# Performance work log

Hardware: AMD Instinct MI355X
Metric: run time of the kernel (lower is better)

## Reference

```python
import jax, jax.numpy as jnp
import numpy as np

H = 128          # LSTMCell hidden size (fixed in module)
D_IN = 128       # input_dim
D_PROJ = 256     # input_layer output / LSTM input size
LAYER_NUM = 2
DA = 128
R = 8
OUT_DIM = 7
B = 256
T = 512
TS = 32          # time_steps


def _lstm_cell(h, c, x_t, W_ih, b_ih, W_hh, b_hh):
    # PyTorch LSTMCell gate order: i, f, g, o
    gates = x_t @ W_ih.T + h @ W_hh.T + (b_ih + b_hh)
    i, f, g, o = jnp.split(gates, 4, axis=-1)
    c_new = jax.nn.sigmoid(f) * c + jax.nn.sigmoid(i) * jnp.tanh(g)
    h_new = jax.nn.sigmoid(o) * jnp.tanh(c_new)
    return h_new, c_new


def _chunked_lstm(x_tbd, W_ih, b_ih, W_hh, b_hh, w_time, time_steps):
    # x_tbd: [T, B, 256]. Every `time_steps` steps, h/c are replaced by a
    # learned linear reweighting (time_w_layer) of the buffered chunk states;
    # the chunk's last emitted output is the reweighted h (as in the source).
    Tt, Bb, Dd = x_tbd.shape

    def cell_step(carry, x_t):
        h, c = carry
        h, c = _lstm_cell(h, c, x_t, W_ih, b_ih, W_hh, b_hh)
        return (h, c), (h, c)

    def chunk_step(carry, x_chunk):        # x_chunk: [ts, B, 256]
        _, (hs, cs) = jax.lax.scan(cell_step, carry, x_chunk)  # hs: [ts, B, H]
        h_new = jnp.einsum('t,tbh->bh', w_time, hs)
        c_new = jnp.einsum('t,tbh->bh', w_time, cs)
        return (h_new, c_new), hs.at[-1].set(h_new)

    n_chunks = Tt // time_steps
    x_chunks = x_tbd.reshape(n_chunks, time_steps, Bb, Dd)
    h0 = jnp.zeros((Bb, H), x_tbd.dtype)
    _, outs = jax.lax.scan(chunk_step, (h0, jnp.zeros_like(h0)), x_chunks)
    return outs.reshape(Tt, Bb, H)


def setup_inputs() -> dict:
    key = jax.random.key(0)
    ks = jax.random.split(key, 16)
    def unif(k, shape, fan_in):
        bound = 1.0 / np.sqrt(fan_in)
        return jax.random.uniform(k, shape, jnp.float32, -bound, bound)
    inp = {
        'x': jax.random.normal(ks[0], (B, T, D_IN), jnp.float32),
        'W_in': unif(ks[1], (D_PROJ, D_IN), D_IN),
        'b_in': unif(ks[2], (D_PROJ,), D_IN),
        'W_ih': unif(ks[3], (4 * H, D_PROJ), H),
        'b_ih': unif(ks[4], (4 * H,), H),
        'W_hh': unif(ks[5], (4 * H, H), H),
        'b_hh': unif(ks[6], (4 * H,), H),
        'w_time': unif(ks[7], (TS,), TS),
        'W_a1': unif(ks[8], (DA, 2 * H), 2 * H),
        'b_a1': unif(ks[9], (DA,), 2 * H),
        'W_a2': unif(ks[10], (R, DA), DA),
        'W_out': unif(ks[11], (OUT_DIM, 2 * H * R), 2 * H * R),
        'b_out': unif(ks[12], (OUT_DIM,), 2 * H * R),
        'length': jax.random.randint(ks[13], (B,), T // 2, T + 1),
        'batch_size': B,
        'time_steps': TS,
        'r': R,
    }
    return inp


def reference(x, W_in, b_in, W_ih, b_ih, W_hh, b_hh, w_time, W_a1, b_a1,
              W_a2, W_out, b_out, length, batch_size, time_steps, r):
    Bb, Tt, _ = x.shape
    out = x @ W_in.T + b_in                       # [B, T, 256]
    for _ in range(LAYER_NUM):                    # shared LSTM weights per source
        inp = jnp.transpose(out, (1, 0, 2))       # [T, B, 256]
        out1 = _chunked_lstm(inp, W_ih, b_ih, W_hh, b_hh, w_time, time_steps)
        out2 = _chunked_lstm(inp[::-1], W_ih, b_ih, W_hh, b_hh, w_time, time_steps)
        # NOTE: backward outputs are NOT re-reversed (faithful to source)
        out = jnp.transpose(jnp.concatenate([out1, out2], axis=-1), (1, 0, 2))
    # attention (dropout = identity at eval)
    pot = jnp.tanh(out @ W_a1.T + b_a1) @ W_a2.T  # [B, T, r]
    mask = (jnp.arange(Tt)[None, :] < length[:, None])[:, :, None]
    logits = jnp.where(mask, pot, -jnp.inf)
    weight = jnp.where(mask, jax.nn.softmax(logits, axis=1), 0.0)  # [B, T, r]
    wT = jnp.transpose(weight, (0, 2, 1))          # [B, r, T]
    pooled = jnp.einsum('brt,bth->brh', wT, out).reshape(Bb, -1)   # [B, r*256]
    out_final = jax.nn.log_softmax(pooled @ W_out.T + b_out, axis=1)
    sw = jnp.sqrt(wT)
    gram = jnp.einsum('brt,bst->brs', sw, sw)      # [B, r, r]
    penalty = jnp.sum((gram - 1.0) ** 2)           # oneMat is all-ones
    return out_final, penalty
```

## Files before the change

### kernel.cpp

```cpp
#include <hip/hip_runtime.h>
#include <math.h>

namespace {

constexpr int Bb = 256, Tt = 512, Dp = 256, Hh = 128, G = 512;
constexpr int M = Tt * Bb;

typedef __attribute__((ext_vector_type(8))) short short8v;
typedef __attribute__((ext_vector_type(4))) float f32x4;

__device__ __forceinline__ float sigf(float x) {
  return __builtin_amdgcn_rcpf(1.0f + __expf(-x));
}
__device__ __forceinline__ float tanhfast(float x) {
  const float e = __expf(2.0f * x);
  return 1.0f - 2.0f * __builtin_amdgcn_rcpf(e + 1.0f);
}
__device__ __forceinline__ float b2f(unsigned short u) {
  return __uint_as_float((unsigned int)u << 16);
}
__device__ __forceinline__ unsigned short f2b(float f) {
  unsigned int u = __float_as_uint(f);
  u += 0x7FFFu + ((u >> 16) & 1u);
  return (unsigned short)(u >> 16);
}
__device__ __forceinline__ unsigned int pack2(float a, float b) {
  return (unsigned int)f2b(a) | ((unsigned int)f2b(b) << 16);
}
__device__ __forceinline__ void gload16(const unsigned short* g, unsigned short* l) {
  __builtin_amdgcn_global_load_lds(
      (const __attribute__((address_space(1))) unsigned int*)g,
      (__attribute__((address_space(3))) unsigned int*)l, 16, 0, 0);
}
__device__ __forceinline__ void block_sync_lds() {
  __builtin_amdgcn_sched_barrier(0);
  asm volatile("s_waitcnt lgkmcnt(0)" ::: "memory");
  __builtin_amdgcn_s_barrier();
  __builtin_amdgcn_sched_barrier(0);
}

__global__ __launch_bounds__(256) void wconv_k(const float* __restrict__ src,
                                               unsigned short* __restrict__ dst) {
  const int i = (blockIdx.x * 256 + threadIdx.x) * 4;
  const float4 v = *reinterpret_cast<const float4*>(src + i);
  uint2 o; o.x = pack2(v.x, v.y); o.y = pack2(v.z, v.w);
  *reinterpret_cast<uint2*>(dst + i) = o;
}

__global__ __launch_bounds__(256) void xconv_k(const float* __restrict__ x,
                                               unsigned short* __restrict__ out) {
  const int tid = threadIdx.x;
  const int m = blockIdx.x * 8 + (tid >> 5);
  const int t = m >> 8, b = m & 255;
  const int c4 = (tid & 31) * 4;
  const float4 v = *reinterpret_cast<const float4*>(x + ((size_t)b * Tt + t) * 128 + c4);
  uint2 o; o.x = pack2(v.x, v.y); o.y = pack2(v.z, v.w);
  *reinterpret_cast<uint2*>(out + (size_t)m * 128 + c4) = o;
}

template<int K, int POT, typename CT>
__global__ __launch_bounds__(256) void mgemm_k(const unsigned short* __restrict__ A,
    const unsigned short* __restrict__ W, const float* __restrict__ bias1,
    const float* __restrict__ bias2, const float* __restrict__ Wa2,
    CT* __restrict__ C, int N) {
  constexpr int NK = K / 64;
  __shared__ unsigned short smem[32768];
  unsigned short* aLds = smem;
  unsigned short* wLds = smem + 16384;
  const int tid = threadIdx.x;
  const int lane = tid & 63;
  const int wave = tid >> 6;
  const int wm = wave >> 1, wn = wave & 1;
  const int m0 = blockIdx.y * 128, n0 = blockIdx.x * 128;
  const int lrow = lane & 15, lk8 = (lane >> 4) * 8;

  const unsigned short* Ab = A + (size_t)(m0 + lrow) * K + lk8;
  const unsigned short* Wb = W + (size_t)(n0 + lrow) * K + lk8;

  auto stage = [&](int buf, int kb) {
#pragma unroll
    for (int i = 0; i < 4; ++i) {
      const int c = wave * 4 + i, f = c & 7, kc = c >> 3;
      const size_t go = (size_t)(f * 16) * K + kb * 64 + kc * 32;
      gload16(Ab + go, &aLds[buf * 8192 + c * 512]);
      gload16(Wb + go, &wLds[buf * 8192 + c * 512]);
    }
  };

  f32x4 acc[4][4] = {};
  stage(0, 0);
  __syncthreads();
  int cur = 0;
  for (int kb = 0; kb < NK; ++kb) {
    if (kb + 1 < NK) stage(cur ^ 1, kb + 1);
#pragma unroll
    for (int kc = 0; kc < 2; ++kc) {
      short8v af[4], bfr[4];
#pragma unroll
      for (int i = 0; i < 4; ++i)
        af[i] = *reinterpret_cast<const short8v*>(
            &aLds[cur * 8192 + ((kc * 8 + wm * 4 + i) * 64 + lane) * 8]);
#pragma unroll
      for (int j = 0; j < 4; ++j)
        bfr[j] = *reinterpret_cast<const short8v*>(
            &wLds[cur * 8192 + ((kc * 8 + wn * 4 + j) * 64 + lane) * 8]);
#pragma unroll
      for (int i = 0; i < 4; ++i)
#pragma unroll
        for (int j = 0; j < 4; ++j)
          acc[i][j] = __builtin_amdgcn_mfma_f32_16x16x32_bf16(af[i], bfr[j], acc[i][j], 0, 0, 0);
    }
    __syncthreads();
    cur ^= 1;
  }

  if constexpr (POT) {
    unsigned short* pt = smem;
#pragma unroll
    for (int j = 0; j < 4; ++j) {
      const int coln = wn * 64 + j * 16 + (lane & 15);
      const float bv = bias1[coln];
#pragma unroll
      for (int i = 0; i < 4; ++i) {
        const int rown = wm * 64 + i * 16 + ((lane >> 4) << 2);
#pragma unroll
        for (int r = 0; r < 4; ++r)
          pt[(rown + r) * 136 + coln] = f2b(tanhfast(acc[i][j][r] + bv));
      }
    }
    __syncthreads();
    short8v wfr[4];
#pragma unroll
    for (int ks = 0; ks < 4; ++ks) {
      short8v f = {0, 0, 0, 0, 0, 0, 0, 0};
      if (lrow < 8) {
        const float* src = Wa2 + lrow * 128 + ks * 32 + lk8;
        const float4 a = *reinterpret_cast<const float4*>(src);
        const float4 b = *reinterpret_cast<const float4*>(src + 4);
        f[0] = (short)f2b(a.x); f[1] = (short)f2b(a.y);
        f[2] = (short)f2b(a.z); f[3] = (short)f2b(a.w);
        f[4] = (short)f2b(b.x); f[5] = (short)f2b(b.y);
        f[6] = (short)f2b(b.z); f[7] = (short)f2b(b.w);
      }
      wfr[ks] = f;
    }
    float* pot = reinterpret_cast<float*>(C);
#pragma unroll
    for (int ff = 0; ff < 2; ++ff) {
      const int fr = wave * 2 + ff;
      f32x4 pacc = {0.f, 0.f, 0.f, 0.f};
#pragma unroll
      for (int ks = 0; ks < 4; ++ks) {
        const short8v af = *reinterpret_cast<const short8v*>(
            &pt[(fr * 16 + lrow) * 136 + ks * 32 + lk8]);
        pacc = __builtin_amdgcn_mfma_f32_16x16x32_bf16(af, wfr[ks], pacc, 0, 0, 0);
      }
      if ((lane & 15) < 8) {
#pragma unroll
        for (int r = 0; r < 4; ++r)
          pot[(size_t)(m0 + fr * 16 + ((lane >> 4) << 2) + r) * 8 + (lane & 15)] = pacc[r];
      }
    }
  } else {
#pragma unroll
    for (int j = 0; j < 4; ++j) {
      const int gn = n0 + wn * 64 + j * 16 + (lane & 15);
      float bv = bias1[gn];
      if (bias2) bv += bias2[gn];
#pragma unroll
      for (int i = 0; i < 4; ++i) {
        const int gmb = m0 + wm * 64 + i * 16 + ((lane >> 4) << 2);
#pragma unroll
        for (int r = 0; r < 4; ++r) {
          const float v = acc[i][j][r] + bv;
          const size_t oidx = (size_t)(gmb + r) * N + gn;
          if constexpr (sizeof(CT) == 2) C[oidx] = f2b(v); else C[oidx] = v;
        }
      }
    }
  }
}

__global__ __launch_bounds__(512, 2) void lstm_k(const unsigned short* __restrict__ P,
    const float* __restrict__ Whh, const float* __restrict__ wtime,
    unsigned short* __restrict__ Y) {
  const int tid = threadIdx.x;
  const int lane = tid & 63;
  const int w = tid >> 6;
  const int u = lane & 15;
  const int q = lane >> 4;
  const int dir = blockIdx.x >> 7;
  const int b0 = (blockIdx.x & 127) * 2;

  __shared__ unsigned short hbuf[2][2048];
  __shared__ unsigned int pgbuf[2][512];
  __shared__ unsigned short histb[4096];
  __shared__ float wts[32];

  short8v bfrag[4][4];
#pragma unroll
  for (int gt = 0; gt < 4; ++gt) {
    const int col = gt * 128 + w * 16 + u;
#pragma unroll
    for (int ks = 0; ks < 4; ++ks) {
      const int k0 = ks * 32 + q * 8;
      const float4 w0 = *reinterpret_cast<const float4*>(Whh + (size_t)col * 128 + k0);
      const float4 w1 = *reinterpret_cast<const float4*>(Whh + (size_t)col * 128 + k0 + 4);
      short8v f;
      f[0] = (short)f2b(w0.x); f[1] = (short)f2b(w0.y);
      f[2] = (short)f2b(w0.z); f[3] = (short)f2b(w0.w);
      f[4] = (short)f2b(w1.x); f[5] = (short)f2b(w1.y);
      f[6] = (short)f2b(w1.z); f[7] = (short)f2b(w1.w);
      bfrag[gt][ks] = f;
    }
  }

  for (int i = tid; i < 2048; i += 512) { hbuf[0][i] = 0; hbuf[1][i] = 0; }
  if (tid < 32) wts[tid] = wtime[tid];
  const unsigned int* P32 = reinterpret_cast<const unsigned int*>(P);
  const int prow = tid >> 8, pword = tid & 255;
  const size_t pthread = (size_t)(b0 + prow) * 256 + pword;
  const ptrdiff_t dstep = (dir ? -(ptrdiff_t)1 : (ptrdiff_t)1) * (ptrdiff_t)(Bb * 256);
  unsigned int np_h1 = 0, np_h2 = 0;
  {
    const int t0 = dir ? (Tt - 1) : 0;
    pgbuf[0][tid] = P32[(size_t)t0 * Bb * 256 + pthread];
    const int t1 = dir ? (Tt - 2) : 1;
    np_h1 = P32[(size_t)t1 * Bb * 256 + pthread];
    const int t2 = dir ? (Tt - 3) : 2;
    np_h2 = P32[(size_t)t2 * Bb * 256 + pthread];
  }
  ptrdiff_t poff = (ptrdiff_t)((size_t)(dir ? (Tt - 4) : 3) * Bb * 256 + pthread);
  const int r_own = q & 1;
  const int colh = w * 16 + u;
  float c_st = 0.f, ha = 0.f, ca = 0.f;
  __syncthreads();

  auto body = [&](int s, int cur) {
    unsigned int np_new = 0;
    if (s < Tt - 3) np_new = P32[poff];
    short8v afrag[4];
#pragma unroll
    for (int ks = 0; ks < 4; ++ks)
      afrag[ks] = *reinterpret_cast<const short8v*>(&hbuf[cur][(ks * 4 + q) * 128 + u * 8]);
    f32x4 gacc[4];
#pragma unroll
    for (int gt = 0; gt < 4; ++gt) {
      f32x4 acc = {0.f, 0.f, 0.f, 0.f};
#pragma unroll
      for (int ks = 0; ks < 4; ++ks)
        acc = __builtin_amdgcn_mfma_f32_16x16x32_bf16(afrag[ks], bfrag[gt][ks], acc, 0, 0, 0);
      gacc[gt] = acc;
    }
    if (s + 1 < Tt) pgbuf[cur ^ 1][tid] = np_h1;
    if (lane < 32) {
      const float wt = wts[s & 31];
      float g4[4];
#pragma unroll
      for (int gt = 0; gt < 4; ++gt) {
        const unsigned int pw = pgbuf[cur][r_own * 256 + gt * 64 + (colh >> 1)];
        const unsigned short pb = (colh & 1) ? (unsigned short)(pw >> 16)
                                             : (unsigned short)(pw & 0xFFFF);
        g4[gt] = gacc[gt][0] + b2f(pb);
      }
      float cs = sigf(g4[1]) * c_st + sigf(g4[0]) * tanhfast(g4[2]);
      float hn = sigf(g4[3]) * tanhfast(cs);
      ha += wt * hn;
      ca += wt * cs;
      if ((s & 31) == 31) { hn = ha; cs = ca; ha = 0.f; ca = 0.f; }
      c_st = cs;
      const unsigned short hb = f2b(hn);
      hbuf[cur ^ 1][(colh >> 3) * 128 + r_own * 32 + (colh & 7)] = hb;
      histb[((s & 15) * 2 + r_own) * 128 + colh] = hb;
    }
    if ((s & 7) == 0 && s) {
      const int k = tid >> 6, r2 = (tid >> 5) & 1, c4 = (tid & 31) * 4;
      const int bs = s - 8;
      const uint2 v = *reinterpret_cast<const uint2*>(
          &histb[(((bs + k) & 15) * 2 + r2) * 128 + c4]);
      *reinterpret_cast<uint2*>(
          &Y[((size_t)(bs + k) * Bb + b0 + r2) * Dp + dir * Hh + c4]) = v;
    }
    block_sync_lds();
    np_h1 = np_h2;
    np_h2 = np_new;
    poff += dstep;
  };

  for (int s = 0; s < Tt; s += 2) {
    body(s, 0);
    body(s + 1, 1);
  }
  {
    const int k = tid >> 6, r2 = (tid >> 5) & 1, c4 = (tid & 31) * 4;
    const int bs = Tt - 8;
    const uint2 v = *reinterpret_cast<const uint2*>(
        &histb[(((bs + k) & 15) * 2 + r2) * 128 + c4]);
    *reinterpret_cast<uint2*>(
        &Y[((size_t)(bs + k) * Bb + b0 + r2) * Dp + dir * Hh + c4]) = v;
  }
}

__global__ __launch_bounds__(256) void softmax_k(const float* __restrict__ pot,
    const int* __restrict__ length, float* __restrict__ Wt) {
  const int b = blockIdx.x >> 3, r = blockIdx.x & 7;
  const int tid = threadIdx.x;
  const int len = length[b];
  __shared__ float rbuf[4];
  const int t1 = tid, t2 = tid + 256;
  const float x1 = (t1 < len) ? pot[((size_t)t1 * Bb + b) * 8 + r] : -INFINITY;
  const float x2 = (t2 < len) ? pot[((size_t)t2 * Bb + b) * 8 + r] : -INFINITY;
  float m = fmaxf(x1, x2);
#pragma unroll
  for (int off = 32; off >= 1; off >>= 1) m = fmaxf(m, __shfl_xor(m, off));
  if ((tid & 63) == 0) rbuf[tid >> 6] = m;
  __syncthreads();
  m = fmaxf(fmaxf(rbuf[0], rbuf[1]), fmaxf(rbuf[2], rbuf[3]));
  const float e1 = (t1 < len) ? __expf(x1 - m) : 0.f;
  const float e2 = (t2 < len) ? __expf(x2 - m) : 0.f;
  float ssum = e1 + e2;
#pragma unroll
  for (int off = 32; off >= 1; off >>= 1) ssum += __shfl_xor(ssum, off);
  __syncthreads();
  if ((tid & 63) == 0) rbuf[tid >> 6] = ssum;
  __syncthreads();
  ssum = rbuf[0] + rbuf[1] + rbuf[2] + rbuf[3];
  const float inv = 1.0f / ssum;
  float* wrow = Wt + ((size_t)b * 8 + r) * Tt;
  wrow[t1] = e1 * inv;
  wrow[t2] = e2 * inv;
}

__global__ __launch_bounds__(256) void pool_k(const unsigned short* __restrict__ Y,
    const float* __restrict__ Wt, const float* __restrict__ Wout,
    const float* __restrict__ bout, float* __restrict__ outF,
    float* __restrict__ penpart) {
  const int b = blockIdx.x;
  const int tid = threadIdx.x;
  __shared__ float ws[8 * 513];
  __shared__ float pooled[2048];
  __shared__ float red[256];
  __shared__ float lg[8];
  for (int i = tid; i < 4096; i += 256) ws[(i >> 9) * 513 + (i & 511)] = Wt[(size_t)b * 4096 + i];
  __syncthreads();
  float acc[8] = {};
  for (int t = 0; t < Tt; ++t) {
    const float y = b2f(Y[((size_t)t * Bb + b) * Dp + tid]);
#pragma unroll
    for (int r = 0; r < 8; ++r) acc[r] += ws[r * 513 + t] * y;
  }
#pragma unroll
  for (int r = 0; r < 8; ++r) pooled[r * 256 + tid] = acc[r];
  __syncthreads();
  for (int o = 0; o < 7; ++o) {
    float p = 0.f;
    for (int j = tid; j < 2048; j += 256) p += pooled[j] * Wout[(size_t)o * 2048 + j];
    red[tid] = p;
    __syncthreads();
    for (int st = 128; st >= 1; st >>= 1) {
      if (tid < st) red[tid] += red[tid + st];
      __syncthreads();
    }
    if (tid == 0) lg[o] = red[0] + bout[o];
    __syncthreads();
  }
  if (tid == 0) {
    float mx = lg[0];
    for (int o = 1; o < 7; ++o) mx = fmaxf(mx, lg[o]);
    float ssum = 0.f;
    for (int o = 0; o < 7; ++o) ssum += __expf(lg[o] - mx);
    const float lse = mx + __logf(ssum);
    for (int o = 0; o < 7; ++o) outF[b * 7 + o] = lg[o] - lse;
  }
  for (int i = tid; i < 4096; i += 256) {
    const int rr = i >> 9, t = i & 511;
    ws[rr * 513 + t] = sqrtf(ws[rr * 513 + t]);
  }
  __syncthreads();
  float pp = 0.f;
  if (tid < 64) {
    const int rr = tid >> 3, ssi = tid & 7;
    float g = 0.f;
    for (int t = 0; t < Tt; ++t) g += ws[rr * 513 + t] * ws[ssi * 513 + t];
    const float d = g - 1.0f;
    pp = d * d;
  }
  red[tid] = pp;
  __syncthreads();
  for (int st = 128; st >= 1; st >>= 1) {
    if (tid < st) red[tid] += red[tid + st];
    __syncthreads();
  }
  if (tid == 0) penpart[b] = red[0];
}

__global__ __launch_bounds__(256) void penred_k(const float* __restrict__ penpart,
                                                float* __restrict__ outp) {
  const int tid = threadIdx.x;
  __shared__ float red[256];
  red[tid] = penpart[tid];
  __syncthreads();
  for (int st = 128; st >= 1; st >>= 1) {
    if (tid < st) red[tid] += red[tid + st];
    __syncthreads();
  }
  if (tid == 0) outp[0] = red[0];
}

}

extern "C" void kernel_launch(void* const* d_in, const int* in_sizes, int n_in,
                              void* d_out, int out_size, void* d_ws, size_t ws_size,
                              hipStream_t stream) {
  (void)in_sizes; (void)n_in; (void)out_size;
  const float* x     = (const float*)d_in[0];
  const float* W_in  = (const float*)d_in[1];
  const float* b_in  = (const float*)d_in[2];
  const float* W_ih  = (const float*)d_in[3];
  const float* b_ih  = (const float*)d_in[4];
  const float* W_hh  = (const float*)d_in[5];
  const float* b_hh  = (const float*)d_in[6];
  const float* wtime = (const float*)d_in[7];
  const float* W_a1  = (const float*)d_in[8];
  const float* b_a1  = (const float*)d_in[9];
  const float* W_a2  = (const float*)d_in[10];
  const float* W_out = (const float*)d_in[11];
  const float* b_out = (const float*)d_in[12];
  const int*   length= (const int*)d_in[13];
  float* outF = (float*)d_out;

  typedef unsigned short bf16;
  char* ws = (char*)d_ws;
  size_t off = 0;
  auto alloc = [&](size_t bytes) {
    void* p = ws + off; off += (bytes + 255) & ~(size_t)255; return p;
  };
  bf16*  act  = (bf16*)alloc((size_t)M * 256 * 2);
  bf16*  Pg   = (bf16*)alloc((size_t)M * 512 * 2);
  bf16*  xb   = (bf16*)alloc((size_t)M * 128 * 2);
  float* pot  = (float*)alloc((size_t)M * 8 * 4);
  float* Wt   = (float*)alloc((size_t)Bb * 8 * Tt * 4);
  float* penp = (float*)alloc(Bb * 4);
  bf16*  Wihb = (bf16*)alloc(512 * 256 * 2);
  bf16*  Winb = (bf16*)alloc(256 * 128 * 2);
  bf16*  Wa1b = (bf16*)alloc(128 * 256 * 2);

  if (ws_size < off) return;

  const dim3 blk(256);
  wconv_k<<<dim3(32),  blk, 0, stream>>>(W_in, Winb);
  wconv_k<<<dim3(128), blk, 0, stream>>>(W_ih, Wihb);
  wconv_k<<<dim3(32),  blk, 0, stream>>>(W_a1, Wa1b);
  xconv_k<<<dim3(M / 8), blk, 0, stream>>>(x, xb);
  mgemm_k<128, 0, bf16><<<dim3(2, M / 128), blk, 0, stream>>>(xb, Winb, b_in, nullptr, nullptr, act, 256);
  mgemm_k<256, 0, bf16><<<dim3(4, M / 128), blk, 0, stream>>>(act, Wihb, b_ih, b_hh, nullptr, Pg, 512);
  lstm_k<<<dim3(256), dim3(512), 0, stream>>>(Pg, W_hh, wtime, act);
  mgemm_k<256, 0, bf16><<<dim3(4, M / 128), blk, 0, stream>>>(act, Wihb, b_ih, b_hh, nullptr, Pg, 512);
  lstm_k<<<dim3(256), dim3(512), 0, stream>>>(Pg, W_hh, wtime, act);
  mgemm_k<256, 1, float><<<dim3(1, M / 128), blk, 0, stream>>>(act, Wa1b, b_a1, nullptr, W_a2, pot, 128);
  softmax_k<<<dim3(Bb * 8), blk, 0, stream>>>(pot, length, Wt);
  pool_k<<<dim3(Bb), blk, 0, stream>>>(act, Wt, W_out, b_out, outF, penp);
  penred_k<<<dim3(1), blk, 0, stream>>>(penp, outF + Bb * 7);
}
```

Baseline: 898.0 us.

## Split LSTM recurrence to one batch row per block, doubling grid size

The recurrent LSTM kernel now handles one batch row per block instead of two, launching 512 blocks rather than 256, and the launch bound is raised to 4 blocks per SU. Per-step LDS buffers shrink, and only the first 16 lanes of each wave do the gate math. The goal is to spread the serial recurrence across more CUs so each block's per-step critical path is shorter. The cost is that every block still runs the full 16x16 MFMA tile while using only one of its rows, and each block reloads the W_hh fragments, so MFMA work and weight loading roughly double. Register pressure under the tighter launch bound could also cause spills.

```diff
diff --git a/kernel.cpp b/kernel.cpp
--- a/kernel.cpp
+++ b/kernel.cpp
@@ -181,7 +181,7 @@
   }
 }
 
-__global__ __launch_bounds__(512, 2) void lstm_k(const unsigned short* __restrict__ P,
+__global__ __launch_bounds__(512, 4) void lstm_k(const unsigned short* __restrict__ P,
     const float* __restrict__ Whh, const float* __restrict__ wtime,
     unsigned short* __restrict__ Y) {
   const int tid = threadIdx.x;
@@ -189,12 +189,12 @@
   const int w = tid >> 6;
   const int u = lane & 15;
   const int q = lane >> 4;
-  const int dir = blockIdx.x >> 7;
-  const int b0 = (blockIdx.x & 127) * 2;
+  const int dir = blockIdx.x >> 8;
+  const int b0 = blockIdx.x & 255;
 
   __shared__ unsigned short hbuf[2][2048];
-  __shared__ unsigned int pgbuf[2][512];
-  __shared__ unsigned short histb[4096];
+  __shared__ unsigned int pgbuf[2][256];
+  __shared__ unsigned short histb[2048];
   __shared__ float wts[32];
 
   short8v bfrag[4][4];
@@ -218,11 +218,11 @@
   for (int i = tid; i < 2048; i += 512) { hbuf[0][i] = 0; hbuf[1][i] = 0; }
   if (tid < 32) wts[tid] = wtime[tid];
   const unsigned int* P32 = reinterpret_cast<const unsigned int*>(P);
-  const int prow = tid >> 8, pword = tid & 255;
-  const size_t pthread = (size_t)(b0 + prow) * 256 + pword;
+  const bool pf = tid < 256;
+  const size_t pthread = (size_t)b0 * 256 + tid;
   const ptrdiff_t dstep = (dir ? -(ptrdiff_t)1 : (ptrdiff_t)1) * (ptrdiff_t)(Bb * 256);
   unsigned int np_h1 = 0, np_h2 = 0;
-  {
+  if (pf) {
     const int t0 = dir ? (Tt - 1) : 0;
     pgbuf[0][tid] = P32[(size_t)t0 * Bb * 256 + pthread];
     const int t1 = dir ? (Tt - 2) : 1;
@@ -231,14 +231,13 @@
     np_h2 = P32[(size_t)t2 * Bb * 256 + pthread];
   }
   ptrdiff_t poff = (ptrdiff_t)((size_t)(dir ? (Tt - 4) : 3) * Bb * 256 + pthread);
-  const int r_own = q & 1;
   const int colh = w * 16 + u;
   float c_st = 0.f, ha = 0.f, ca = 0.f;
   __syncthreads();
 
   auto body = [&](int s, int cur) {
     unsigned int np_new = 0;
-    if (s < Tt - 3) np_new = P32[poff];
+    if (pf && s < Tt - 3) np_new = P32[poff];
     short8v afrag[4];
 #pragma unroll
     for (int ks = 0; ks < 4; ++ks)
@@ -252,13 +251,13 @@
         acc = __builtin_amdgcn_mfma_f32_16x16x32_bf16(afrag[ks], bfrag[gt][ks], acc, 0, 0, 0);
       gacc[gt] = acc;
     }
-    if (s + 1 < Tt) pgbuf[cur ^ 1][tid] = np_h1;
-    if (lane < 32) {
+    if (pf && s + 1 < Tt) pgbuf[cur ^ 1][tid] = np_h1;
+    if (lane < 16) {
       const float wt = wts[s & 31];
       float g4[4];
 #pragma unroll
       for (int gt = 0; gt < 4; ++gt) {
-        const unsigned int pw = pgbuf[cur][r_own * 256 + gt * 64 + (colh >> 1)];
+        const unsigned int pw = pgbuf[cur][gt * 64 + (colh >> 1)];
         const unsigned short pb = (colh & 1) ? (unsigned short)(pw >> 16)
                                              : (unsigned short)(pw & 0xFFFF);
         g4[gt] = gacc[gt][0] + b2f(pb);
@@ -270,16 +269,15 @@
       if ((s & 31) == 31) { hn = ha; cs = ca; ha = 0.f; ca = 0.f; }
       c_st = cs;
       const unsigned short hb = f2b(hn);
-      hbuf[cur ^ 1][(colh >> 3) * 128 + r_own * 32 + (colh & 7)] = hb;
-      histb[((s & 15) * 2 + r_own) * 128 + colh] = hb;
-    }
-    if ((s & 7) == 0 && s) {
-      const int k = tid >> 6, r2 = (tid >> 5) & 1, c4 = (tid & 31) * 4;
+      hbuf[cur ^ 1][(colh >> 3) * 128 + (colh & 7)] = hb;
+      histb[(s & 15) * 128 + colh] = hb;
+    }
+    if ((s & 7) == 0 && s && pf) {
+      const int k = tid >> 5, c4 = (tid & 31) * 4;
       const int bs = s - 8;
-      const uint2 v = *reinterpret_cast<const uint2*>(
-          &histb[(((bs + k) & 15) * 2 + r2) * 128 + c4]);
+      const uint2 v = *reinterpret_cast<const uint2*>(&histb[((bs + k) & 15) * 128 + c4]);
       *reinterpret_cast<uint2*>(
-          &Y[((size_t)(bs + k) * Bb + b0 + r2) * Dp + dir * Hh + c4]) = v;
+          &Y[((size_t)(bs + k) * Bb + b0) * Dp + dir * Hh + c4]) = v;
     }
     block_sync_lds();
     np_h1 = np_h2;
@@ -292,12 +290,13 @@
     body(s + 1, 1);
   }
   {
-    const int k = tid >> 6, r2 = (tid >> 5) & 1, c4 = (tid & 31) * 4;
-    const int bs = Tt - 8;
-    const uint2 v = *reinterpret_cast<const uint2*>(
-        &histb[(((bs + k) & 15) * 2 + r2) * 128 + c4]);
-    *reinterpret_cast<uint2*>(
-        &Y[((size_t)(bs + k) * Bb + b0 + r2) * Dp + dir * Hh + c4]) = v;
+    if (pf) {
+      const int k = tid >> 5, c4 = (tid & 31) * 4;
+      const int bs = Tt - 8;
+      const uint2 v = *reinterpret_cast<const uint2*>(&histb[((bs + k) & 15) * 128 + c4]);
+      *reinterpret_cast<uint2*>(
+          &Y[((size_t)(bs + k) * Bb + b0) * Dp + dir * Hh + c4]) = v;
+    }
   }
 }
 
@@ -454,9 +453,9 @@
   xconv_k<<<dim3(M / 8), blk, 0, stream>>>(x, xb);
   mgemm_k<128, 0, bf16><<<dim3(2, M / 128), blk, 0, stream>>>(xb, Winb, b_in, nullptr, nullptr, act, 256);
   mgemm_k<256, 0, bf16><<<dim3(4, M / 128), blk, 0, stream>>>(act, Wihb, b_ih, b_hh, nullptr, Pg, 512);
-  lstm_k<<<dim3(256), dim3(512), 0, stream>>>(Pg, W_hh, wtime, act);
+  lstm_k<<<dim3(512), dim3(512), 0, stream>>>(Pg, W_hh, wtime, act);
   mgemm_k<256, 0, bf16><<<dim3(4, M / 128), blk, 0, stream>>>(act, Wihb, b_ih, b_hh, nullptr, Pg, 512);
-  lstm_k<<<dim3(256), dim3(512), 0, stream>>>(Pg, W_hh, wtime, act);
+  lstm_k<<<dim3(512), dim3(512), 0, stream>>>(Pg, W_hh, wtime, act);
   mgemm_k<256, 1, float><<<dim3(1, M / 128), blk, 0, stream>>>(act, Wa1b, b_a1, nullptr, W_a2, pot, 128);
   softmax_k<<<dim3(Bb * 8), blk, 0, stream>>>(pot, length, Wt);
   pool_k<<<dim3(Bb), blk, 0, stream>>>(act, Wt, W_out, b_out, outF, penp);
```

New measurement: 1.227 ms. 36.7% more time.

## Halve LSTM block to 4 waves, each computing two 16-column tiles

Applied to the files above, without the earlier changes.

The recurrent LSTM kernel now runs 256 threads per block instead of 512. Each wave keeps W_hh fragments for two 16-column tiles and issues twice as many MFMAs per step, and all 64 lanes do the gate math instead of only half. The aim is to shrink the per-step block barrier and make better use of lanes on the latency-bound serial recurrence. In exchange, each wave holds twice as many register-resident weight fragments, which raises register pressure and lengthens each wave's serial MFMA chain.

```diff
diff --git a/kernel.cpp b/kernel.cpp
--- a/kernel.cpp
+++ b/kernel.cpp
@@ -181,7 +181,7 @@
   }
 }
 
-__global__ __launch_bounds__(512, 2) void lstm_k(const unsigned short* __restrict__ P,
+__global__ __launch_bounds__(256, 2) void lstm_k(const unsigned short* __restrict__ P,
     const float* __restrict__ Whh, const float* __restrict__ wtime,
     unsigned short* __restrict__ Y) {
   const int tid = threadIdx.x;
@@ -197,71 +197,82 @@
   __shared__ unsigned short histb[4096];
   __shared__ float wts[32];
 
-  short8v bfrag[4][4];
-#pragma unroll
-  for (int gt = 0; gt < 4; ++gt) {
-    const int col = gt * 128 + w * 16 + u;
-#pragma unroll
-    for (int ks = 0; ks < 4; ++ks) {
-      const int k0 = ks * 32 + q * 8;
-      const float4 w0 = *reinterpret_cast<const float4*>(Whh + (size_t)col * 128 + k0);
-      const float4 w1 = *reinterpret_cast<const float4*>(Whh + (size_t)col * 128 + k0 + 4);
-      short8v f;
-      f[0] = (short)f2b(w0.x); f[1] = (short)f2b(w0.y);
-      f[2] = (short)f2b(w0.z); f[3] = (short)f2b(w0.w);
-      f[4] = (short)f2b(w1.x); f[5] = (short)f2b(w1.y);
-      f[6] = (short)f2b(w1.z); f[7] = (short)f2b(w1.w);
-      bfrag[gt][ks] = f;
-    }
-  }
-
-  for (int i = tid; i < 2048; i += 512) { hbuf[0][i] = 0; hbuf[1][i] = 0; }
+  short8v bfrag[4][2][4];
+#pragma unroll
+  for (int gt = 0; gt < 4; ++gt)
+#pragma unroll
+    for (int t2 = 0; t2 < 2; ++t2) {
+      const int col = gt * 128 + w * 32 + t2 * 16 + u;
+#pragma unroll
+      for (int ks = 0; ks < 4; ++ks) {
+        const int k0 = ks * 32 + q * 8;
+        const float4 w0 = *reinterpret_cast<const float4*>(Whh + (size_t)col * 128 + k0);
+        const float4 w1 = *reinterpret_cast<const float4*>(Whh + (size_t)col * 128 + k0 + 4);
+        short8v f;
+        f[0] = (short)f2b(w0.x); f[1] = (short)f2b(w0.y);
+        f[2] = (short)f2b(w0.z); f[3] = (short)f2b(w0.w);
+        f[4] = (short)f2b(w1.x); f[5] = (short)f2b(w1.y);
+        f[6] = (short)f2b(w1.z); f[7] = (short)f2b(w1.w);
+        bfrag[gt][t2][ks] = f;
+      }
+    }
+
+  for (int i = tid; i < 2048; i += 256) { hbuf[0][i] = 0; hbuf[1][i] = 0; }
   if (tid < 32) wts[tid] = wtime[tid];
   const unsigned int* P32 = reinterpret_cast<const unsigned int*>(P);
-  const int prow = tid >> 8, pword = tid & 255;
-  const size_t pthread = (size_t)(b0 + prow) * 256 + pword;
-  const ptrdiff_t dstep = (dir ? -(ptrdiff_t)1 : (ptrdiff_t)1) * (ptrdiff_t)(Bb * 256);
-  unsigned int np_h1 = 0, np_h2 = 0;
+  const size_t bstep = (size_t)Bb * 256;
+  const ptrdiff_t pstep = dir ? -(ptrdiff_t)bstep : (ptrdiff_t)bstep;
+  const size_t b0w = (size_t)b0 * 256 + tid;
+  const size_t b1w = (size_t)(b0 + 1) * 256 + tid;
+  ptrdiff_t pt0 = (ptrdiff_t)((size_t)(dir ? (Tt - 1) : 0) * bstep);
+  unsigned int h1a, h1b, h2a, h2b;
   {
-    const int t0 = dir ? (Tt - 1) : 0;
-    pgbuf[0][tid] = P32[(size_t)t0 * Bb * 256 + pthread];
-    const int t1 = dir ? (Tt - 2) : 1;
-    np_h1 = P32[(size_t)t1 * Bb * 256 + pthread];
-    const int t2 = dir ? (Tt - 3) : 2;
-    np_h2 = P32[(size_t)t2 * Bb * 256 + pthread];
-  }
-  ptrdiff_t poff = (ptrdiff_t)((size_t)(dir ? (Tt - 4) : 3) * Bb * 256 + pthread);
-  const int r_own = q & 1;
-  const int colh = w * 16 + u;
+    pgbuf[0][tid] = P32[pt0 + b0w];
+    pgbuf[0][tid + 256] = P32[pt0 + b1w];
+    h1a = P32[pt0 + pstep + b0w];
+    h1b = P32[pt0 + pstep + b1w];
+    h2a = P32[pt0 + 2 * pstep + b0w];
+    h2b = P32[pt0 + 2 * pstep + b1w];
+  }
+  ptrdiff_t poff = pt0 + 3 * pstep;
+  const int t2o = lane >> 5;
+  const int r_own = (lane >> 4) & 1;
+  const int colh = w * 32 + t2o * 16 + u;
   float c_st = 0.f, ha = 0.f, ca = 0.f;
   __syncthreads();
 
   auto body = [&](int s, int cur) {
-    unsigned int np_new = 0;
-    if (s < Tt - 3) np_new = P32[poff];
+    unsigned int na = 0, nb = 0;
+    if (s < Tt - 3) { na = P32[poff + b0w]; nb = P32[poff + b1w]; }
     short8v afrag[4];
 #pragma unroll
     for (int ks = 0; ks < 4; ++ks)
       afrag[ks] = *reinterpret_cast<const short8v*>(&hbuf[cur][(ks * 4 + q) * 128 + u * 8]);
-    f32x4 gacc[4];
-#pragma unroll
-    for (int gt = 0; gt < 4; ++gt) {
-      f32x4 acc = {0.f, 0.f, 0.f, 0.f};
-#pragma unroll
-      for (int ks = 0; ks < 4; ++ks)
-        acc = __builtin_amdgcn_mfma_f32_16x16x32_bf16(afrag[ks], bfrag[gt][ks], acc, 0, 0, 0);
-      gacc[gt] = acc;
-    }
-    if (s + 1 < Tt) pgbuf[cur ^ 1][tid] = np_h1;
-    if (lane < 32) {
+    f32x4 gacc[4][2];
+#pragma unroll
+    for (int gt = 0; gt < 4; ++gt)
+#pragma unroll
+      for (int t2 = 0; t2 < 2; ++t2) {
+        f32x4 acc = {0.f, 0.f, 0.f, 0.f};
+#pragma unroll
+        for (int ks = 0; ks < 4; ++ks)
+          acc = __builtin_amdgcn_mfma_f32_16x16x32_bf16(afrag[ks], bfrag[gt][t2][ks], acc, 0, 0, 0);
+        gacc[gt][t2] = acc;
+      }
+    if (s + 1 < Tt) {
+      pgbuf[cur ^ 1][tid] = h1a;
+      pgbuf[cur ^ 1][tid + 256] = h1b;
+    }
+    {
       const float wt = wts[s & 31];
       float g4[4];
 #pragma unroll
       for (int gt = 0; gt < 4; ++gt) {
+        const float gv = t2o ? gacc[gt][1][0] : gacc[gt][0][0];
         const unsigned int pw = pgbuf[cur][r_own * 256 + gt * 64 + (colh >> 1)];
         const unsigned short pb = (colh & 1) ? (unsigned short)(pw >> 16)
                                              : (unsigned short)(pw & 0xFFFF);
-        g4[gt] = gacc[gt][0] + b2f(pb);
+        g4[gt] = gv + b2f(pb);
       }
       float cs = sigf(g4[1]) * c_st + sigf(g4[0]) * tanhfast(g4[2]);
       float hn = sigf(g4[3]) * tanhfast(cs);
@@ -274,17 +285,17 @@
       histb[((s & 15) * 2 + r_own) * 128 + colh] = hb;
     }
     if ((s & 7) == 0 && s) {
-      const int k = tid >> 6, r2 = (tid >> 5) & 1, c4 = (tid & 31) * 4;
+      const int k = tid >> 5, r2 = (tid >> 4) & 1, c8 = (tid & 15) * 8;
       const int bs = s - 8;
-      const uint2 v = *reinterpret_cast<const uint2*>(
-          &histb[(((bs + k) & 15) * 2 + r2) * 128 + c4]);
-      *reinterpret_cast<uint2*>(
-          &Y[((size_t)(bs + k) * Bb + b0 + r2) * Dp + dir * Hh + c4]) = v;
+      const uint4 v = *reinterpret_cast<const uint4*>(
+          &histb[(((bs + k) & 15) * 2 + r2) * 128 + c8]);
+      *reinterpret_cast<uint4*>(
+          &Y[((size_t)(bs + k) * Bb + b0 + r2) * Dp + dir * Hh + c8]) = v;
     }
     block_sync_lds();
-    np_h1 = np_h2;
-    np_h2 = np_new;
-    poff += dstep;
+    h1a = h2a; h1b = h2b;
+    h2a = na;  h2b = nb;
+    poff += pstep;
   };
 
   for (int s = 0; s < Tt; s += 2) {
@@ -292,12 +303,12 @@
     body(s + 1, 1);
   }
   {
-    const int k = tid >> 6, r2 = (tid >> 5) & 1, c4 = (tid & 31) * 4;
+    const int k = tid >> 5, r2 = (tid >> 4) & 1, c8 = (tid & 15) * 8;
     const int bs = Tt - 8;
-    const uint2 v = *reinterpret_cast<const uint2*>(
-        &histb[(((bs + k) & 15) * 2 + r2) * 128 + c4]);
-    *reinterpret_cast<uint2*>(
-        &Y[((size_t)(bs + k) * Bb + b0 + r2) * Dp + dir * Hh + c4]) = v;
+    const uint4 v = *reinterpret_cast<const uint4*>(
+        &histb[(((bs + k) & 15) * 2 + r2) * 128 + c8]);
+    *reinterpret_cast<uint4*>(
+        &Y[((size_t)(bs + k) * Bb + b0 + r2) * Dp + dir * Hh + c8]) = v;
   }
 }
 
@@ -454,9 +465,9 @@
   xconv_k<<<dim3(M / 8), blk, 0, stream>>>(x, xb);
   mgemm_k<128, 0, bf16><<<dim3(2, M / 128), blk, 0, stream>>>(xb, Winb, b_in, nullptr, nullptr, act, 256);
   mgemm_k<256, 0, bf16><<<dim3(4, M / 128), blk, 0, stream>>>(act, Wihb, b_ih, b_hh, nullptr, Pg, 512);
-  lstm_k<<<dim3(256), dim3(512), 0, stream>>>(Pg, W_hh, wtime, act);
+  lstm_k<<<dim3(256), blk, 0, stream>>>(Pg, W_hh, wtime, act);
   mgemm_k<256, 0, bf16><<<dim3(4, M / 128), blk, 0, stream>>>(act, Wihb, b_ih, b_hh, nullptr, Pg, 512);
-  lstm_k<<<dim3(256), dim3(512), 0, stream>>>(Pg, W_hh, wtime, act);
+  lstm_k<<<dim3(256), blk, 0, stream>>>(Pg, W_hh, wtime, act);
   mgemm_k<256, 1, float><<<dim3(1, M / 128), blk, 0, stream>>>(act, Wa1b, b_a1, nullptr, W_a2, pot, 128);
   softmax_k<<<dim3(Bb * 8), blk, 0, stream>>>(pot, length, Wt);
   pool_k<<<dim3(Bb), blk, 0, stream>>>(act, Wt, W_out, b_out, outF, penp);
```

Result: slower. 953.5 us (+6.2%).
